# Kernel optimization log

Hardware: AMD Instinct MI355X
Metric: run time of the kernel (lower is better)

The kernel has to match this reference:

```python
import jax, jax.numpy as jnp
import numpy as np
from jax import lax

DT = 1.0  # self.dt


def setup_inputs() -> dict:
    key = jax.random.key(0)
    k1, k2 = jax.random.split(key)
    B, T, D = 16, 4096, 512
    x = jax.random.normal(k1, (B, T, D), dtype=jnp.float32)
    W = jax.random.normal(k2, (D,), dtype=jnp.float32)  # CustomLinearLayer.weight
    return {"x": x, "W": W}


def reference(x, W):
    # w = exp(-exp(W)) - 1 in (-1, 0]; w_res = sqrt(1 - w^2)
    w = jnp.exp(-jnp.exp(W)) - 1.0          # [D]
    w_res = jnp.sqrt(1.0 - w * w)           # [D]
    a = 1.0 + DT * w                        # decay factor per channel, [D]
    b = DT * w_res                          # input scale per channel, [D]

    # h_{t+1} = h_t + dt * (h_t * w + x_t * w_res) = a * h_t + b * x_t
    bx = x * b                              # [B, T, D] (fused elementwise)
    xt = jnp.swapaxes(bx, 0, 1)             # [T, B, D] scan over time

    def step(h, u):
        h_next = a * h + u
        return h_next, h_next

    h0 = jnp.zeros(x.shape[:1] + x.shape[2:], dtype=x.dtype)  # [B, D]
    _, hs = lax.scan(step, h0, xt)          # hs: [T, B, D]
    return jnp.swapaxes(hs, 0, 1)           # [B, T, D] (return_sequences=True)
```

## Files before the change

kernel.cpp:

```cpp
#include <hip/hip_runtime.h>


#define BB 16
#define TT 4096
#define DD 512
#define KK 64
#define LL (TT / KK)
#define D4 (DD / 4)

__device__ __forceinline__ void coeffs(const float* __restrict__ W, int d,
                                       float& a0, float& a1, float& a2, float& a3,
                                       float& b0, float& b1, float& b2, float& b3) {
    float w;
    w = expf(-expf(W[d + 0])) - 1.0f; a0 = 1.0f + w; b0 = sqrtf(1.0f - w * w);
    w = expf(-expf(W[d + 1])) - 1.0f; a1 = 1.0f + w; b1 = sqrtf(1.0f - w * w);
    w = expf(-expf(W[d + 2])) - 1.0f; a2 = 1.0f + w; b2 = sqrtf(1.0f - w * w);
    w = expf(-expf(W[d + 3])) - 1.0f; a3 = 1.0f + w; b3 = sqrtf(1.0f - w * w);
}

__global__ __launch_bounds__(D4) void lru_phase1(const float4* __restrict__ x,
                                                 const float* __restrict__ W,
                                                 float4* __restrict__ E) {
    const int d4 = threadIdx.x;
    const int k  = blockIdx.x;
    const int b  = blockIdx.y;
    const int d  = d4 * 4;

    float a0, a1, a2, a3, b0, b1, b2, b3;
    coeffs(W, d, a0, a1, a2, a3, b0, b1, b2, b3);

    const float4* xp = x + ((size_t)b * TT + (size_t)k * LL) * D4 + d4;
    float h0 = 0.f, h1 = 0.f, h2 = 0.f, h3 = 0.f;
#pragma unroll 8
    for (int i = 0; i < LL; ++i) {
        float4 v = xp[(size_t)i * D4];
        h0 = a0 * h0 + b0 * v.x;
        h1 = a1 * h1 + b1 * v.y;
        h2 = a2 * h2 + b2 * v.z;
        h3 = a3 * h3 + b3 * v.w;
    }
    E[((size_t)b * KK + k) * D4 + d4] = make_float4(h0, h1, h2, h3);
}

__global__ __launch_bounds__(D4) void lru_phase2(const float* __restrict__ W,
                                                 float4* __restrict__ E) {
    const int d4 = threadIdx.x;
    const int b  = blockIdx.x;
    const int d  = d4 * 4;

    float a0, a1, a2, a3, b0, b1, b2, b3;
    coeffs(W, d, a0, a1, a2, a3, b0, b1, b2, b3);

    float aL0 = a0, aL1 = a1, aL2 = a2, aL3 = a3;
#pragma unroll
    for (int s = 0; s < 6; ++s) { aL0 *= aL0; aL1 *= aL1; aL2 *= aL2; aL3 *= aL3; }

    float c0 = 0.f, c1 = 0.f, c2 = 0.f, c3 = 0.f;
    for (int k = 0; k < KK; ++k) {
        size_t idx = ((size_t)b * KK + k) * D4 + d4;
        float4 e = E[idx];
        E[idx] = make_float4(c0, c1, c2, c3);
        c0 = aL0 * c0 + e.x;
        c1 = aL1 * c1 + e.y;
        c2 = aL2 * c2 + e.z;
        c3 = aL3 * c3 + e.w;
    }
}

__global__ __launch_bounds__(D4) void lru_phase3(const float4* __restrict__ x,
                                                 const float* __restrict__ W,
                                                 const float4* __restrict__ C,
                                                 float4* __restrict__ out) {
    const int d4 = threadIdx.x;
    const int k  = blockIdx.x;
    const int b  = blockIdx.y;
    const int d  = d4 * 4;

    float a0, a1, a2, a3, b0, b1, b2, b3;
    coeffs(W, d, a0, a1, a2, a3, b0, b1, b2, b3);

    float4 c = C[((size_t)b * KK + k) * D4 + d4];
    float h0 = c.x, h1 = c.y, h2 = c.z, h3 = c.w;

    const size_t base = ((size_t)b * TT + (size_t)k * LL) * D4 + d4;
    const float4* xp = x + base;
    float4* op = out + base;
#pragma unroll 8
    for (int i = 0; i < LL; ++i) {
        float4 v = xp[(size_t)i * D4];
        h0 = a0 * h0 + b0 * v.x;
        h1 = a1 * h1 + b1 * v.y;
        h2 = a2 * h2 + b2 * v.z;
        h3 = a3 * h3 + b3 * v.w;
        op[(size_t)i * D4] = make_float4(h0, h1, h2, h3);
    }
}

extern "C" void kernel_launch(void* const* d_in, const int* in_sizes, int n_in,
                              void* d_out, int out_size, void* d_ws, size_t ws_size,
                              hipStream_t stream) {
    const float4* x = (const float4*)d_in[0];
    const float*  W = (const float*)d_in[1];
    float4* out = (float4*)d_out;
    float4* E   = (float4*)d_ws;

    dim3 grid(KK, BB);
    dim3 block(D4);
    lru_phase1<<<grid, block, 0, stream>>>(x, W, E);
    lru_phase2<<<dim3(BB), dim3(D4), 0, stream>>>(W, E);
    lru_phase3<<<grid, block, 0, stream>>>(x, W, E, out);
}
```

Before: 260.2 us.

## Replace three-phase chunked scan with single-pass decoupled look-back scan

The three kernels (chunk reduce, carry scan, rescan) become one kernel. Each block takes a dynamic tile id from an atomic counter, scans a 16-step chunk held in registers, publishes its local aggregate and then its inclusive prefix through flags, and resolves its carry by looking back over predecessors. This reads x once instead of twice and drops the serial middle kernel. The cost is spin-waiting on flags, agent-scope atomic loads and stores, a small init kernel to zero the counter and flags, and reliance on dynamic tile ordering for forward progress.

```diff
diff --git a/kernel.cpp b/kernel.cpp
--- a/kernel.cpp
+++ b/kernel.cpp
@@ -4,95 +4,123 @@
 #define BB 16
 #define TT 4096
 #define DD 512
-#define KK 64
-#define LL (TT / KK)
+#define LL 16
+#define KK (TT / LL)
+#define NT (BB * KK)
 #define D4 (DD / 4)
 
-__device__ __forceinline__ void coeffs(const float* __restrict__ W, int d,
-                                       float& a0, float& a1, float& a2, float& a3,
-                                       float& b0, float& b1, float& b2, float& b3) {
-    float w;
-    w = expf(-expf(W[d + 0])) - 1.0f; a0 = 1.0f + w; b0 = sqrtf(1.0f - w * w);
-    w = expf(-expf(W[d + 1])) - 1.0f; a1 = 1.0f + w; b1 = sqrtf(1.0f - w * w);
-    w = expf(-expf(W[d + 2])) - 1.0f; a2 = 1.0f + w; b2 = sqrtf(1.0f - w * w);
-    w = expf(-expf(W[d + 3])) - 1.0f; a3 = 1.0f + w; b3 = sqrtf(1.0f - w * w);
+#define WS_FLAGS_OFF 1024
+#define WS_E_OFF     32768
+#define WS_P_OFF     (WS_E_OFF + NT * DD * 4)
+
+__device__ __forceinline__ float aload(const float* p) {
+    return __hip_atomic_load(p, __ATOMIC_RELAXED, __HIP_MEMORY_SCOPE_AGENT);
+}
+__device__ __forceinline__ void astore(float* p, float v) {
+    __hip_atomic_store(p, v, __ATOMIC_RELAXED, __HIP_MEMORY_SCOPE_AGENT);
 }
 
-__global__ __launch_bounds__(D4) void lru_phase1(const float4* __restrict__ x,
-                                                 const float* __restrict__ W,
-                                                 float4* __restrict__ E) {
-    const int d4 = threadIdx.x;
-    const int k  = blockIdx.x;
-    const int b  = blockIdx.y;
-    const int d  = d4 * 4;
-
-    float a0, a1, a2, a3, b0, b1, b2, b3;
-    coeffs(W, d, a0, a1, a2, a3, b0, b1, b2, b3);
-
-    const float4* xp = x + ((size_t)b * TT + (size_t)k * LL) * D4 + d4;
-    float h0 = 0.f, h1 = 0.f, h2 = 0.f, h3 = 0.f;
-#pragma unroll 8
-    for (int i = 0; i < LL; ++i) {
-        float4 v = xp[(size_t)i * D4];
-        h0 = a0 * h0 + b0 * v.x;
-        h1 = a1 * h1 + b1 * v.y;
-        h2 = a2 * h2 + b2 * v.z;
-        h3 = a3 * h3 + b3 * v.w;
-    }
-    E[((size_t)b * KK + k) * D4 + d4] = make_float4(h0, h1, h2, h3);
+__global__ __launch_bounds__(256) void lru_init(int* ws) {
+    int i = blockIdx.x * blockDim.x + threadIdx.x;
+    if (i < WS_E_OFF / 4) ws[i] = 0;
 }
 
-__global__ __launch_bounds__(D4) void lru_phase2(const float* __restrict__ W,
-                                                 float4* __restrict__ E) {
-    const int d4 = threadIdx.x;
-    const int b  = blockIdx.x;
-    const int d  = d4 * 4;
+__global__ __launch_bounds__(D4) void lru_scan(const float4* __restrict__ x,
+                                               const float* __restrict__ W,
+                                               float4* __restrict__ out,
+                                               int* __restrict__ counter,
+                                               int* __restrict__ flags,
+                                               float* __restrict__ E,
+                                               float* __restrict__ P) {
+    __shared__ int s_tile;
+    __shared__ int s_flag;
+    const int tid = threadIdx.x;
+    if (tid == 0) s_tile = atomicAdd(counter, 1);
+    __syncthreads();
+    const int tile = s_tile;
+    const int b = tile & (BB - 1);
+    const int k = tile >> 4;
+    const int d = tid * 4;
 
-    float a0, a1, a2, a3, b0, b1, b2, b3;
-    coeffs(W, d, a0, a1, a2, a3, b0, b1, b2, b3);
-
+    float e, w;
+    e = expf(-expf(W[d + 0])); const float a0 = e; w = e - 1.0f; const float bb0 = sqrtf(1.0f - w * w);
+    e = expf(-expf(W[d + 1])); const float a1 = e; w = e - 1.0f; const float bb1 = sqrtf(1.0f - w * w);
+    e = expf(-expf(W[d + 2])); const float a2 = e; w = e - 1.0f; const float bb2 = sqrtf(1.0f - w * w);
+    e = expf(-expf(W[d + 3])); const float a3 = e; w = e - 1.0f; const float bb3 = sqrtf(1.0f - w * w);
     float aL0 = a0, aL1 = a1, aL2 = a2, aL3 = a3;
 #pragma unroll
-    for (int s = 0; s < 6; ++s) { aL0 *= aL0; aL1 *= aL1; aL2 *= aL2; aL3 *= aL3; }
+    for (int s = 0; s < 4; ++s) { aL0 *= aL0; aL1 *= aL1; aL2 *= aL2; aL3 *= aL3; }
+
+    const size_t base = ((size_t)b * TT + (size_t)k * LL) * D4 + tid;
+    float4 h[LL];
+    float h0 = 0.f, h1 = 0.f, h2 = 0.f, h3 = 0.f;
+#pragma unroll
+    for (int i = 0; i < LL; ++i) {
+        float4 v = x[base + (size_t)i * D4];
+        h0 = a0 * h0 + bb0 * v.x;
+        h1 = a1 * h1 + bb1 * v.y;
+        h2 = a2 * h2 + bb2 * v.z;
+        h3 = a3 * h3 + bb3 * v.w;
+        h[i] = make_float4(h0, h1, h2, h3);
+    }
 
     float c0 = 0.f, c1 = 0.f, c2 = 0.f, c3 = 0.f;
-    for (int k = 0; k < KK; ++k) {
-        size_t idx = ((size_t)b * KK + k) * D4 + d4;
-        float4 e = E[idx];
-        E[idx] = make_float4(c0, c1, c2, c3);
-        c0 = aL0 * c0 + e.x;
-        c1 = aL1 * c1 + e.y;
-        c2 = aL2 * c2 + e.z;
-        c3 = aL3 * c3 + e.w;
+    float* Erow = E + (size_t)tile * DD + d;
+    float* Prow = P + (size_t)tile * DD + d;
+
+    if (k == 0) {
+        astore(Prow + 0, h0); astore(Prow + 1, h1);
+        astore(Prow + 2, h2); astore(Prow + 3, h3);
+        __syncthreads();
+        if (tid == 0)
+            __hip_atomic_store(&flags[tile], 2, __ATOMIC_RELEASE, __HIP_MEMORY_SCOPE_AGENT);
+    } else {
+        astore(Erow + 0, h0); astore(Erow + 1, h1);
+        astore(Erow + 2, h2); astore(Erow + 3, h3);
+        __syncthreads();
+        if (tid == 0)
+            __hip_atomic_store(&flags[tile], 1, __ATOMIC_RELEASE, __HIP_MEMORY_SCOPE_AGENT);
+
+        float s0 = 1.f, s1 = 1.f, s2 = 1.f, s3 = 1.f;
+        for (int j = k - 1; j >= 0; --j) {
+            const int jt = (j << 4) | b;
+            if (tid == 0) {
+                int f;
+                for (;;) {
+                    f = __hip_atomic_load(&flags[jt], __ATOMIC_ACQUIRE, __HIP_MEMORY_SCOPE_AGENT);
+                    if (f != 0) break;
+                    __builtin_amdgcn_s_sleep(1);
+                }
+                s_flag = f;
+            }
+            __syncthreads();
+            const int f = s_flag;
+            __syncthreads();
+            const float* src = (f == 2) ? (P + (size_t)jt * DD + d)
+                                        : (E + (size_t)jt * DD + d);
+            float v0 = aload(src + 0), v1 = aload(src + 1);
+            float v2 = aload(src + 2), v3 = aload(src + 3);
+            c0 += s0 * v0; c1 += s1 * v1; c2 += s2 * v2; c3 += s3 * v3;
+            if (f == 2) break;
+            s0 *= aL0; s1 *= aL1; s2 *= aL2; s3 *= aL3;
+        }
+
+        astore(Prow + 0, h0 + aL0 * c0);
+        astore(Prow + 1, h1 + aL1 * c1);
+        astore(Prow + 2, h2 + aL2 * c2);
+        astore(Prow + 3, h3 + aL3 * c3);
+        __syncthreads();
+        if (tid == 0)
+            __hip_atomic_store(&flags[tile], 2, __ATOMIC_RELEASE, __HIP_MEMORY_SCOPE_AGENT);
     }
-}
 
-__global__ __launch_bounds__(D4) void lru_phase3(const float4* __restrict__ x,
-                                                 const float* __restrict__ W,
-                                                 const float4* __restrict__ C,
-                                                 float4* __restrict__ out) {
-    const int d4 = threadIdx.x;
-    const int k  = blockIdx.x;
-    const int b  = blockIdx.y;
-    const int d  = d4 * 4;
-
-    float a0, a1, a2, a3, b0, b1, b2, b3;
-    coeffs(W, d, a0, a1, a2, a3, b0, b1, b2, b3);
-
-    float4 c = C[((size_t)b * KK + k) * D4 + d4];
-    float h0 = c.x, h1 = c.y, h2 = c.z, h3 = c.w;
-
-    const size_t base = ((size_t)b * TT + (size_t)k * LL) * D4 + d4;
-    const float4* xp = x + base;
-    float4* op = out + base;
-#pragma unroll 8
+    float s0 = a0, s1 = a1, s2 = a2, s3 = a3;
+#pragma unroll
     for (int i = 0; i < LL; ++i) {
-        float4 v = xp[(size_t)i * D4];
-        h0 = a0 * h0 + b0 * v.x;
-        h1 = a1 * h1 + b1 * v.y;
-        h2 = a2 * h2 + b2 * v.z;
-        h3 = a3 * h3 + b3 * v.w;
-        op[(size_t)i * D4] = make_float4(h0, h1, h2, h3);
+        float4 o = h[i];
+        o.x += s0 * c0; o.y += s1 * c1; o.z += s2 * c2; o.w += s3 * c3;
+        out[base + (size_t)i * D4] = o;
+        s0 *= a0; s1 *= a1; s2 *= a2; s3 *= a3;
     }
 }
 
@@ -102,11 +130,13 @@
     const float4* x = (const float4*)d_in[0];
     const float*  W = (const float*)d_in[1];
     float4* out = (float4*)d_out;
-    float4* E   = (float4*)d_ws;
 
-    dim3 grid(KK, BB);
-    dim3 block(D4);
-    lru_phase1<<<grid, block, 0, stream>>>(x, W, E);
-    lru_phase2<<<dim3(BB), dim3(D4), 0, stream>>>(W, E);
-    lru_phase3<<<grid, block, 0, stream>>>(x, W, E, out);
+    char* ws = (char*)d_ws;
+    int*   counter = (int*)ws;
+    int*   flags   = (int*)(ws + WS_FLAGS_OFF);
+    float* E       = (float*)(ws + WS_E_OFF);
+    float* P       = (float*)(ws + WS_P_OFF);
+
+    lru_init<<<dim3(WS_E_OFF / 4 / 256), dim3(256), 0, stream>>>((int*)ws);
+    lru_scan<<<dim3(NT), dim3(D4), 0, stream>>>(x, W, out, counter, flags, E, P);
 }
```

New measurement: 949.0 us. +264.7%, slower.

## Double chunk count, pack two chunks per block, nontemporal output stores

Applied to the files above, without the earlier changes.

Raises the number of time chunks from 64 to 128 (chunk length 32), so the first and third phases expose more independent serial work per batch. Each block now handles two chunks through a 2-D thread block. The carry phase writes to a separate buffer instead of updating in place, and the output is written with nontemporal stores to avoid polluting cache. The trade-off is a longer serial carry scan in phase 2 and more workspace memory.

```diff
diff --git a/kernel.cpp b/kernel.cpp
--- a/kernel.cpp
+++ b/kernel.cpp
@@ -4,25 +4,27 @@
 #define BB 16
 #define TT 4096
 #define DD 512
-#define KK 64
+#define KK 128
 #define LL (TT / KK)
 #define D4 (DD / 4)
+
+typedef float vfloat4 __attribute__((ext_vector_type(4)));
 
 __device__ __forceinline__ void coeffs(const float* __restrict__ W, int d,
                                        float& a0, float& a1, float& a2, float& a3,
                                        float& b0, float& b1, float& b2, float& b3) {
-    float w;
-    w = expf(-expf(W[d + 0])) - 1.0f; a0 = 1.0f + w; b0 = sqrtf(1.0f - w * w);
-    w = expf(-expf(W[d + 1])) - 1.0f; a1 = 1.0f + w; b1 = sqrtf(1.0f - w * w);
-    w = expf(-expf(W[d + 2])) - 1.0f; a2 = 1.0f + w; b2 = sqrtf(1.0f - w * w);
-    w = expf(-expf(W[d + 3])) - 1.0f; a3 = 1.0f + w; b3 = sqrtf(1.0f - w * w);
+    float e, w;
+    e = expf(-expf(W[d + 0])); a0 = e; w = e - 1.0f; b0 = sqrtf(1.0f - w * w);
+    e = expf(-expf(W[d + 1])); a1 = e; w = e - 1.0f; b1 = sqrtf(1.0f - w * w);
+    e = expf(-expf(W[d + 2])); a2 = e; w = e - 1.0f; b2 = sqrtf(1.0f - w * w);
+    e = expf(-expf(W[d + 3])); a3 = e; w = e - 1.0f; b3 = sqrtf(1.0f - w * w);
 }
 
-__global__ __launch_bounds__(D4) void lru_phase1(const float4* __restrict__ x,
-                                                 const float* __restrict__ W,
-                                                 float4* __restrict__ E) {
+__global__ __launch_bounds__(256) void lru_phase1(const float4* __restrict__ x,
+                                                  const float* __restrict__ W,
+                                                  float4* __restrict__ E) {
     const int d4 = threadIdx.x;
-    const int k  = blockIdx.x;
+    const int k  = blockIdx.x * 2 + threadIdx.y;
     const int b  = blockIdx.y;
     const int d  = d4 * 4;
 
@@ -43,7 +45,8 @@
 }
 
 __global__ __launch_bounds__(D4) void lru_phase2(const float* __restrict__ W,
-                                                 float4* __restrict__ E) {
+                                                 const float4* __restrict__ E,
+                                                 float4* __restrict__ C) {
     const int d4 = threadIdx.x;
     const int b  = blockIdx.x;
     const int d  = d4 * 4;
@@ -53,13 +56,14 @@
 
     float aL0 = a0, aL1 = a1, aL2 = a2, aL3 = a3;
 #pragma unroll
-    for (int s = 0; s < 6; ++s) { aL0 *= aL0; aL1 *= aL1; aL2 *= aL2; aL3 *= aL3; }
+    for (int s = 0; s < 5; ++s) { aL0 *= aL0; aL1 *= aL1; aL2 *= aL2; aL3 *= aL3; }
 
     float c0 = 0.f, c1 = 0.f, c2 = 0.f, c3 = 0.f;
+    const size_t row = (size_t)b * KK * D4 + d4;
+#pragma unroll 8
     for (int k = 0; k < KK; ++k) {
-        size_t idx = ((size_t)b * KK + k) * D4 + d4;
-        float4 e = E[idx];
-        E[idx] = make_float4(c0, c1, c2, c3);
+        float4 e = E[row + (size_t)k * D4];
+        C[row + (size_t)k * D4] = make_float4(c0, c1, c2, c3);
         c0 = aL0 * c0 + e.x;
         c1 = aL1 * c1 + e.y;
         c2 = aL2 * c2 + e.z;
@@ -67,12 +71,12 @@
     }
 }
 
-__global__ __launch_bounds__(D4) void lru_phase3(const float4* __restrict__ x,
-                                                 const float* __restrict__ W,
-                                                 const float4* __restrict__ C,
-                                                 float4* __restrict__ out) {
+__global__ __launch_bounds__(256) void lru_phase3(const float4* __restrict__ x,
+                                                  const float* __restrict__ W,
+                                                  const float4* __restrict__ C,
+                                                  float4* __restrict__ out) {
     const int d4 = threadIdx.x;
-    const int k  = blockIdx.x;
+    const int k  = blockIdx.x * 2 + threadIdx.y;
     const int b  = blockIdx.y;
     const int d  = d4 * 4;
 
@@ -84,7 +88,7 @@
 
     const size_t base = ((size_t)b * TT + (size_t)k * LL) * D4 + d4;
     const float4* xp = x + base;
-    float4* op = out + base;
+    vfloat4* op = (vfloat4*)(out + base);
 #pragma unroll 8
     for (int i = 0; i < LL; ++i) {
         float4 v = xp[(size_t)i * D4];
@@ -92,7 +96,8 @@
         h1 = a1 * h1 + b1 * v.y;
         h2 = a2 * h2 + b2 * v.z;
         h3 = a3 * h3 + b3 * v.w;
-        op[(size_t)i * D4] = make_float4(h0, h1, h2, h3);
+        vfloat4 o; o.x = h0; o.y = h1; o.z = h2; o.w = h3;
+        __builtin_nontemporal_store(o, &op[(size_t)i * D4]);
     }
 }
 
@@ -102,11 +107,14 @@
     const float4* x = (const float4*)d_in[0];
     const float*  W = (const float*)d_in[1];
     float4* out = (float4*)d_out;
-    float4* E   = (float4*)d_ws;
 
-    dim3 grid(KK, BB);
-    dim3 block(D4);
+    char* ws = (char*)d_ws;
+    float4* E = (float4*)ws;
+    float4* C = (float4*)(ws + (size_t)BB * KK * DD * 4);
+
+    dim3 grid(KK / 2, BB);
+    dim3 block(D4, 2);
     lru_phase1<<<grid, block, 0, stream>>>(x, W, E);
-    lru_phase2<<<dim3(BB), dim3(D4), 0, stream>>>(W, E);
-    lru_phase3<<<grid, block, 0, stream>>>(x, W, E, out);
+    lru_phase2<<<dim3(BB), dim3(D4), 0, stream>>>(W, E, C);
+    lru_phase3<<<grid, block, 0, stream>>>(x, W, C, out);
 }
```

New measurement: 259.6 us. No clear change (-0.2%).
